# Optimization experiments

Hardware: AMD Instinct MI355X
Metric: run time of the kernel (lower is better)

## Reference

```python
import jax, jax.numpy as jnp
import numpy as np


def setup_inputs() -> dict:
    key = jax.random.key(0)
    k1, k2 = jax.random.split(key)
    inp = jax.random.normal(k1, (16, 64, 64, 64), dtype=jnp.float32)  # (B, D, H, W)
    codebook = jax.random.normal(k2, (1024, 64), dtype=jnp.float32)  # (K, D)
    return {"input": inp, "codebook": codebook}


def reference(input, codebook):
    # input: (B, D, *spatial); codebook: (K, D)
    B, D = input.shape[0], input.shape[1]
    spatial = input.shape[2:]
    # move channel dim last, flatten to tokens: (N, D)
    x = jnp.moveaxis(input, 1, -1).reshape(-1, D)
    # squared L2 distances (cdist^2), computed via expansion to avoid (N,K,D)
    x_sq = jnp.sum(x * x, axis=-1, keepdims=True)            # (N, 1)
    e_sq = jnp.sum(codebook * codebook, axis=-1)             # (K,)
    dist = x_sq - 2.0 * (x @ codebook.T) + e_sq              # (N, K)
    idx = jnp.argmin(dist, axis=-1)                          # (N,)
    quantized = jnp.take(codebook, idx, axis=0)              # (N, D)
    # reshape back to (B, *spatial, D) then move D to axis 1
    out = jnp.moveaxis(quantized.reshape((B,) + spatial + (D,)), -1, 1)
    indices = idx.reshape((B,) + spatial)
    return out, indices
```

## Files before the change

kernel.cpp:

```cpp
#include <hip/hip_runtime.h>


typedef _Float16 v8h  __attribute__((ext_vector_type(8)));
typedef float    v16f __attribute__((ext_vector_type(16)));

constexpr int   D         = 64;
constexpr int   K         = 1024;
constexpr int   HW        = 4096;
constexpr int   DHW       = D * HW;
constexpr int   OUT_ELEMS = 16 * DHW;
constexpr float EPS       = 0.04f;


__global__ __launch_bounds__(256) void vq_prep(
    const float* __restrict__ cb, _Float16* __restrict__ CH, float* __restrict__ esq)
{
    const int blk = blockIdx.x, tid = threadIdx.x;
    if (blk < 72) {
        const int gid  = blk * 256 + tid;
        const int lane = gid & 63;
        const int fid  = gid >> 6;
        const int t    = fid / 9;
        const int kc   = fid - 9 * t;
        const int l31  = lane & 31;
        const int lh   = lane >> 5;
        const int cw   = t * 32 + l31;
        v8h h;
        if (kc < 8) {
            const int  kk = kc & 3;
            const bool lo = kc >= 4;
            const float* src = cb + cw * D + kk * 16 + lh * 8;
            #pragma unroll
            for (int j = 0; j < 8; ++j) {
                const float v = -2.0f * src[j];
                const _Float16 vh = (_Float16)v;
                h[j] = lo ? (_Float16)(v - (float)vh) : vh;
            }
        } else {
            #pragma unroll
            for (int j = 0; j < 8; ++j) h[j] = (_Float16)0.0f;
            if (lh == 0) {
                const float4* c4 = (const float4*)(cb + cw * D);
                float a0 = 0.f, a1 = 0.f, a2 = 0.f, a3 = 0.f;
                #pragma unroll
                for (int j = 0; j < 16; ++j) {
                    const float4 c = c4[j];
                    a0 = fmaf(c.x, c.x, a0);
                    a1 = fmaf(c.y, c.y, a1);
                    a2 = fmaf(c.z, c.z, a2);
                    a3 = fmaf(c.w, c.w, a3);
                }
                const float e = (a0 + a1) + (a2 + a3);
                const _Float16 ehi = (_Float16)e;
                h[0] = ehi;
                h[1] = (_Float16)(e - (float)ehi);
            }
        }
        *(v8h*)(CH + (size_t)fid * 512 + lane * 8) = h;
    } else {
        const int cw = (blk - 72) * 256 + tid;
        const float4* c4 = (const float4*)(cb + cw * D);
        float a0 = 0.f, a1 = 0.f, a2 = 0.f, a3 = 0.f;
        #pragma unroll
        for (int j = 0; j < 16; ++j) {
            const float4 c = c4[j];
            a0 = fmaf(c.x, c.x, a0);
            a1 = fmaf(c.y, c.y, a1);
            a2 = fmaf(c.z, c.z, a2);
            a3 = fmaf(c.w, c.w, a3);
        }
        esq[cw] = (a0 + a1) + (a2 + a3);
    }
}

__global__ __launch_bounds__(256, 3) void vq_scan(
    const float* __restrict__ input,
    const float* __restrict__ codebook,
    const _Float16* __restrict__ CH,
    const float* __restrict__ esq,
    float* __restrict__ out)
{
    __shared__ union {
        _Float16 bf[2][4][64][8];
        float    q[64][65];
    } u;
    __shared__ float    s_pv[4][64];
    __shared__ float    s_p2[4][64];
    __shared__ int      s_pk[4][64];
    __shared__ int      s_idx[64];
    __shared__ int      s_list[64];
    __shared__ int      s_cnt;
    __shared__ float    s_xf[64];
    __shared__ float    s_redv[4];
    __shared__ int      s_redk[4];

    const int tid  = threadIdx.x;
    const int lane = tid & 63;
    const int q    = __builtin_amdgcn_readfirstlane(tid >> 6);
    const int lh   = lane >> 5;
    const int tok0 = blockIdx.x * 64;
    const int b    = tok0 >> 12;
    const int hwb  = tok0 & 4095;

    if (tid == 0) s_cnt = 0;

    {
        const float* xb = input + (size_t)b * DHW + hwb;
        #pragma unroll
        for (int pass = 0; pass < 4; ++pass) {
            const int d   = pass * 16 + (tid >> 4);
            const int hw4 = (tid & 15) * 4;
            const float4 v = *(const float4*)(xb + (size_t)d * HW + hw4);
            const float vv[4] = {v.x, v.y, v.z, v.w};
            #pragma unroll
            for (int uu = 0; uu < 4; ++uu) {
                const int tk = hw4 + uu;
                u.bf[tk >> 5][d >> 4][((d >> 3) & 1) * 32 + (tk & 31)][d & 7] =
                    (_Float16)vv[uu];
            }
        }
    }
    __syncthreads();

    v8h bh[2][4];
    #pragma unroll
    for (int ct = 0; ct < 2; ++ct)
        #pragma unroll
        for (int kc = 0; kc < 4; ++kc)
            bh[ct][kc] = *(const v8h*)&u.bf[ct][kc][lane][0];

    v8h b5;
    #pragma unroll
    for (int j = 0; j < 8; ++j) b5[j] = (_Float16)0.0f;
    if (lh == 0) { b5[0] = (_Float16)1.0f; b5[1] = (_Float16)1.0f; }

    v16f Z = {0,0,0,0,0,0,0,0,0,0,0,0,0,0,0,0};
    const float INF = __builtin_huge_valf();
    float bv0 = INF, b20 = INF, bv1 = INF, b21 = INF;
    int   sl0 = 0, sl1 = 0;

    const v8h* Abase = (const v8h*)CH + lane;

    #pragma unroll 2
    for (int t = 0; t < 8; ++t) {
        const v8h* Ap = Abase + (size_t)((q * 8 + t) * 9) * 64;
        v8h ah[4], al[4];
        #pragma unroll
        for (int kc = 0; kc < 4; ++kc) {
            ah[kc] = Ap[kc * 64];
            al[kc] = Ap[(kc + 4) * 64];
        }
        const v8h ae = Ap[512];

        v16f acc0 = __builtin_amdgcn_mfma_f32_32x32x16_f16(ae, b5, Z, 0, 0, 0);
        v16f acc1 = __builtin_amdgcn_mfma_f32_32x32x16_f16(ae, b5, Z, 0, 0, 0);

        #pragma unroll
        for (int kc = 0; kc < 4; ++kc) {
            acc0 = __builtin_amdgcn_mfma_f32_32x32x16_f16(ah[kc], bh[0][kc], acc0, 0, 0, 0);
            acc1 = __builtin_amdgcn_mfma_f32_32x32x16_f16(ah[kc], bh[1][kc], acc1, 0, 0, 0);
        }
        #pragma unroll
        for (int kc = 0; kc < 4; ++kc) {
            acc0 = __builtin_amdgcn_mfma_f32_32x32x16_f16(al[kc], bh[0][kc], acc0, 0, 0, 0);
            acc1 = __builtin_amdgcn_mfma_f32_32x32x16_f16(al[kc], bh[1][kc], acc1, 0, 0, 0);
        }

        #pragma unroll
        for (int r = 0; r < 16; ++r) {
            const int slot = (t << 4) | r;
            const float s0 = acc0[r];
            b20 = __builtin_amdgcn_fmed3f(s0, bv0, b20);
            if (s0 < bv0) { bv0 = s0; sl0 = slot; }
            const float s1 = acc1[r];
            b21 = __builtin_amdgcn_fmed3f(s1, bv1, b21);
            if (s1 < bv1) { bv1 = s1; sl1 = slot; }
        }
    }

    #pragma unroll
    for (int ct = 0; ct < 2; ++ct) {
        const float bv = ct ? bv1 : bv0;
        const float b2 = ct ? b21 : b20;
        const int   sl = ct ? sl1 : sl0;
        const float obv = __shfl_xor(bv, 32, 64);
        const float ob2 = __shfl_xor(b2, 32, 64);
        const int   osl = __shfl_xor(sl, 32, 64);
        const bool  oth = obv < bv;
        const float B1  = oth ? obv : bv;
        const float B2  = fminf(fmaxf(bv, obv), fminf(b2, ob2));
        const int   wsl = oth ? osl : sl;
        const int   wlh = oth ? (lh ^ 1) : lh;
        const int   r   = wsl & 15;
        const int   tt  = wsl >> 4;
        const int   cw  = (q * 8 + tt) * 32 + (r & 3) + 8 * (r >> 2) + 4 * wlh;
        if (lane < 32) {
            s_pv[q][ct * 32 + lane] = B1;
            s_p2[q][ct * 32 + lane] = B2;
            s_pk[q][ct * 32 + lane] = cw;
        }
    }
    __syncthreads();

    if (tid < 64) {
        float B1 = INF, B2 = INF; int CW = 0;
        #pragma unroll
        for (int qq = 0; qq < 4; ++qq) {
            const float pv = s_pv[qq][tid];
            const float p2 = s_p2[qq][tid];
            const int   pk = s_pk[qq][tid];
            if (pv < B1) { B2 = fminf(B1, p2); B1 = pv; CW = pk; }
            else         { B2 = fminf(B2, pv); }
        }
        s_idx[tid] = CW;
        if (B2 - B1 < EPS) {
            const int p = atomicAdd(&s_cnt, 1);
            s_list[p] = tid;
        }
    }
    __syncthreads();

    {
        const int cnt = s_cnt;
        const int rr  = tid >> 2;
        const int c   = tid & 3;
        for (int ii = 0; ii < cnt; ++ii) {
            const int tl = s_list[ii];
            if (tid < 64) s_xf[tid] = input[(size_t)b * DHW + (size_t)tid * HW + (hwb + tl)];
            __syncthreads();
            const float4* xs4 = (const float4*)&s_xf[c * 16];
            const float4 x0 = xs4[0], x1 = xs4[1], x2 = xs4[2], x3 = xs4[3];
            float bestv = INF; int bestk = K;
            #pragma unroll 4
            for (int i = 0; i < 16; ++i) {
                const int k = i * 64 + rr;
                const float4* c4 = (const float4*)(codebook + (size_t)k * D + c * 16);
                const float4 c0 = c4[0], c1 = c4[1], c2 = c4[2], c3 = c4[3];
                float p0 = 0.f, p1 = 0.f, p2 = 0.f, p3 = 0.f;
                p0 = fmaf(x0.x, c0.x, p0); p0 = fmaf(x0.y, c0.y, p0);
                p0 = fmaf(x0.z, c0.z, p0); p0 = fmaf(x0.w, c0.w, p0);
                p1 = fmaf(x1.x, c1.x, p1); p1 = fmaf(x1.y, c1.y, p1);
                p1 = fmaf(x1.z, c1.z, p1); p1 = fmaf(x1.w, c1.w, p1);
                p2 = fmaf(x2.x, c2.x, p2); p2 = fmaf(x2.y, c2.y, p2);
                p2 = fmaf(x2.z, c2.z, p2); p2 = fmaf(x2.w, c2.w, p2);
                p3 = fmaf(x3.x, c3.x, p3); p3 = fmaf(x3.y, c3.y, p3);
                p3 = fmaf(x3.z, c3.z, p3); p3 = fmaf(x3.w, c3.w, p3);
                float dp = (p0 + p1) + (p2 + p3);
                dp += __shfl_xor(dp, 1, 64);
                dp += __shfl_xor(dp, 2, 64);
                const float s = fmaf(-2.0f, dp, esq[k]);
                if (s < bestv) { bestv = s; bestk = k; }
            }
            #pragma unroll
            for (int off = 4; off <= 32; off <<= 1) {
                const float ov = __shfl_xor(bestv, off, 64);
                const int   ok = __shfl_xor(bestk, off, 64);
                if (ov < bestv || (ov == bestv && ok < bestk)) { bestv = ov; bestk = ok; }
            }
            if (lane == 0) { s_redv[q] = bestv; s_redk[q] = bestk; }
            __syncthreads();
            if (tid == 0) {
                float bb = s_redv[0]; int bk = s_redk[0];
                #pragma unroll
                for (int w = 1; w < 4; ++w) {
                    const float v = s_redv[w]; const int kk = s_redk[w];
                    if (v < bb || (v == bb && kk < bk)) { bb = v; bk = kk; }
                }
                s_idx[tl] = bk;
            }
            __syncthreads();
        }
    }

    {
        const int rs  = tid >> 2;
        const int c   = tid & 3;
        const int idx = s_idx[rs];
        const float4* src = (const float4*)(codebook + (size_t)idx * D + c * 16);
        #pragma unroll
        for (int j = 0; j < 4; ++j) {
            const float4 v = src[j];
            float* dst = &u.q[rs][c * 16 + j * 4];
            dst[0] = v.x; dst[1] = v.y; dst[2] = v.z; dst[3] = v.w;
        }
    }
    __syncthreads();
    {
        float* ob = out + (size_t)b * DHW + hwb;
        #pragma unroll
        for (int pass = 0; pass < 4; ++pass) {
            const int d   = pass * 16 + (tid >> 4);
            const int hw4 = (tid & 15) * 4;
            float4 v;
            v.x = u.q[hw4 + 0][d];
            v.y = u.q[hw4 + 1][d];
            v.z = u.q[hw4 + 2][d];
            v.w = u.q[hw4 + 3][d];
            *(float4*)(ob + (size_t)d * HW + hw4) = v;
        }
        if (tid < 64) out[OUT_ELEMS + tok0 + tid] = (float)s_idx[tid];
    }
}

extern "C" void kernel_launch(void* const* d_in, const int* in_sizes, int n_in,
                              void* d_out, int out_size, void* d_ws, size_t ws_size,
                              hipStream_t stream) {
    const float* input    = (const float*)d_in[0];
    const float* codebook = (const float*)d_in[1];
    float* out            = (float*)d_out;

    _Float16* CH  = (_Float16*)d_ws;
    float*    esq = (float*)((char*)d_ws + 294912);

    vq_prep<<<76, 256, 0, stream>>>(codebook, CH, esq);
    vq_scan<<<1024, 256, 0, stream>>>(input, codebook, CH, esq, out);
}
```

Before: 120.1 us.

## Double token tile per block, software-pipeline codebook loads, per-wave fallback rescoring

Each scan block now handles 128 tokens instead of 64, so every codebook fragment loaded from global memory feeds four MFMA column groups instead of two, halving codebook traffic per token. The codebook A-fragment loads are double-buffered across tile iterations to overlap with the MFMA work. The exact fp32 fallback for ambiguous tokens now gives each wave its own token with no block-wide barriers per token, and prep folds the esq computation into the fragment pass. The cost is higher register and LDS use, with occupancy hint lowered to 2 blocks per CU and half as many blocks launched.

```diff
diff --git a/kernel.cpp b/kernel.cpp
--- a/kernel.cpp
+++ b/kernel.cpp
@@ -15,65 +15,50 @@
 __global__ __launch_bounds__(256) void vq_prep(
     const float* __restrict__ cb, _Float16* __restrict__ CH, float* __restrict__ esq)
 {
-    const int blk = blockIdx.x, tid = threadIdx.x;
-    if (blk < 72) {
-        const int gid  = blk * 256 + tid;
-        const int lane = gid & 63;
-        const int fid  = gid >> 6;
-        const int t    = fid / 9;
-        const int kc   = fid - 9 * t;
-        const int l31  = lane & 31;
-        const int lh   = lane >> 5;
-        const int cw   = t * 32 + l31;
-        v8h h;
-        if (kc < 8) {
-            const int  kk = kc & 3;
-            const bool lo = kc >= 4;
-            const float* src = cb + cw * D + kk * 16 + lh * 8;
-            #pragma unroll
-            for (int j = 0; j < 8; ++j) {
-                const float v = -2.0f * src[j];
-                const _Float16 vh = (_Float16)v;
-                h[j] = lo ? (_Float16)(v - (float)vh) : vh;
-            }
-        } else {
-            #pragma unroll
-            for (int j = 0; j < 8; ++j) h[j] = (_Float16)0.0f;
-            if (lh == 0) {
-                const float4* c4 = (const float4*)(cb + cw * D);
-                float a0 = 0.f, a1 = 0.f, a2 = 0.f, a3 = 0.f;
-                #pragma unroll
-                for (int j = 0; j < 16; ++j) {
-                    const float4 c = c4[j];
-                    a0 = fmaf(c.x, c.x, a0);
-                    a1 = fmaf(c.y, c.y, a1);
-                    a2 = fmaf(c.z, c.z, a2);
-                    a3 = fmaf(c.w, c.w, a3);
-                }
-                const float e = (a0 + a1) + (a2 + a3);
-                const _Float16 ehi = (_Float16)e;
-                h[0] = ehi;
-                h[1] = (_Float16)(e - (float)ehi);
-            }
-        }
-        *(v8h*)(CH + (size_t)fid * 512 + lane * 8) = h;
+    const int gid  = blockIdx.x * 256 + threadIdx.x;
+    const int lane = gid & 63;
+    const int fid  = gid >> 6;
+    const int t    = fid / 9;
+    const int kc   = fid - 9 * t;
+    const int l31  = lane & 31;
+    const int lh   = lane >> 5;
+    const int cw   = t * 32 + l31;
+    v8h h;
+    if (kc < 8) {
+        const int  kk = kc & 3;
+        const bool lo = kc >= 4;
+        const float* src = cb + cw * D + kk * 16 + lh * 8;
+        #pragma unroll
+        for (int j = 0; j < 8; ++j) {
+            const float v = -2.0f * src[j];
+            const _Float16 vh = (_Float16)v;
+            h[j] = lo ? (_Float16)(v - (float)vh) : vh;
+        }
     } else {
-        const int cw = (blk - 72) * 256 + tid;
-        const float4* c4 = (const float4*)(cb + cw * D);
-        float a0 = 0.f, a1 = 0.f, a2 = 0.f, a3 = 0.f;
-        #pragma unroll
-        for (int j = 0; j < 16; ++j) {
-            const float4 c = c4[j];
-            a0 = fmaf(c.x, c.x, a0);
-            a1 = fmaf(c.y, c.y, a1);
-            a2 = fmaf(c.z, c.z, a2);
-            a3 = fmaf(c.w, c.w, a3);
-        }
-        esq[cw] = (a0 + a1) + (a2 + a3);
-    }
+        #pragma unroll
+        for (int j = 0; j < 8; ++j) h[j] = (_Float16)0.0f;
+        if (lh == 0) {
+            const float4* c4 = (const float4*)(cb + cw * D);
+            float a0 = 0.f, a1 = 0.f, a2 = 0.f, a3 = 0.f;
+            #pragma unroll
+            for (int j = 0; j < 16; ++j) {
+                const float4 c = c4[j];
+                a0 = fmaf(c.x, c.x, a0);
+                a1 = fmaf(c.y, c.y, a1);
+                a2 = fmaf(c.z, c.z, a2);
+                a3 = fmaf(c.w, c.w, a3);
+            }
+            const float e = (a0 + a1) + (a2 + a3);
+            const _Float16 ehi = (_Float16)e;
+            h[0] = ehi;
+            h[1] = (_Float16)(e - (float)ehi);
+            esq[cw] = e;
+        }
+    }
+    *(v8h*)(CH + (size_t)fid * 512 + lane * 8) = h;
 }
 
-__global__ __launch_bounds__(256, 3) void vq_scan(
+__global__ __launch_bounds__(256, 2) void vq_scan(
     const float* __restrict__ input,
     const float* __restrict__ codebook,
     const _Float16* __restrict__ CH,
@@ -81,24 +66,22 @@
     float* __restrict__ out)
 {
     __shared__ union {
-        _Float16 bf[2][4][64][8];
-        float    q[64][65];
+        _Float16 bf[4][4][64][8];
+        float    q[128][65];
     } u;
-    __shared__ float    s_pv[4][64];
-    __shared__ float    s_p2[4][64];
-    __shared__ int      s_pk[4][64];
-    __shared__ int      s_idx[64];
-    __shared__ int      s_list[64];
-    __shared__ int      s_cnt;
-    __shared__ float    s_xf[64];
-    __shared__ float    s_redv[4];
-    __shared__ int      s_redk[4];
+    __shared__ float s_pv[4][128];
+    __shared__ float s_p2[4][128];
+    __shared__ int   s_pk[4][128];
+    __shared__ int   s_idx[128];
+    __shared__ int   s_list[128];
+    __shared__ int   s_cnt;
+    __shared__ float s_xf[4][64];
 
     const int tid  = threadIdx.x;
     const int lane = tid & 63;
     const int q    = __builtin_amdgcn_readfirstlane(tid >> 6);
     const int lh   = lane >> 5;
-    const int tok0 = blockIdx.x * 64;
+    const int tok0 = blockIdx.x * 128;
     const int b    = tok0 >> 12;
     const int hwb  = tok0 & 4095;
 
@@ -107,14 +90,14 @@
     {
         const float* xb = input + (size_t)b * DHW + hwb;
         #pragma unroll
-        for (int pass = 0; pass < 4; ++pass) {
-            const int d   = pass * 16 + (tid >> 4);
-            const int hw4 = (tid & 15) * 4;
-            const float4 v = *(const float4*)(xb + (size_t)d * HW + hw4);
+        for (int pass = 0; pass < 8; ++pass) {
+            const int d   = pass * 8 + (tid >> 5);
+            const int tk4 = (tid & 31) * 4;
+            const float4 v = *(const float4*)(xb + (size_t)d * HW + tk4);
             const float vv[4] = {v.x, v.y, v.z, v.w};
             #pragma unroll
             for (int uu = 0; uu < 4; ++uu) {
-                const int tk = hw4 + uu;
+                const int tk = tk4 + uu;
                 u.bf[tk >> 5][d >> 4][((d >> 3) & 1) * 32 + (tk & 31)][d & 7] =
                     (_Float16)vv[uu];
             }
@@ -122,12 +105,12 @@
     }
     __syncthreads();
 
-    v8h bh[2][4];
+    v8h bh[4][4];
     #pragma unroll
-    for (int ct = 0; ct < 2; ++ct)
+    for (int g = 0; g < 4; ++g)
         #pragma unroll
         for (int kc = 0; kc < 4; ++kc)
-            bh[ct][kc] = *(const v8h*)&u.bf[ct][kc][lane][0];
+            bh[g][kc] = *(const v8h*)&u.bf[g][kc][lane][0];
 
     v8h b5;
     #pragma unroll
@@ -136,73 +119,82 @@
 
     v16f Z = {0,0,0,0,0,0,0,0,0,0,0,0,0,0,0,0};
     const float INF = __builtin_huge_valf();
-    float bv0 = INF, b20 = INF, bv1 = INF, b21 = INF;
-    int   sl0 = 0, sl1 = 0;
+    float bv[4] = {INF, INF, INF, INF};
+    float b2[4] = {INF, INF, INF, INF};
+    int   sl[4] = {0, 0, 0, 0};
 
     const v8h* Abase = (const v8h*)CH + lane;
 
-    #pragma unroll 2
-    for (int t = 0; t < 8; ++t) {
+    v8h ah0[4], al0[4], ae0, ah1[4], al1[4], ae1;
+
+    auto loadA = [&](int t, v8h (&ah)[4], v8h (&al)[4], v8h& ae) {
         const v8h* Ap = Abase + (size_t)((q * 8 + t) * 9) * 64;
-        v8h ah[4], al[4];
         #pragma unroll
         for (int kc = 0; kc < 4; ++kc) {
             ah[kc] = Ap[kc * 64];
             al[kc] = Ap[(kc + 4) * 64];
         }
-        const v8h ae = Ap[512];
-
-        v16f acc0 = __builtin_amdgcn_mfma_f32_32x32x16_f16(ae, b5, Z, 0, 0, 0);
-        v16f acc1 = __builtin_amdgcn_mfma_f32_32x32x16_f16(ae, b5, Z, 0, 0, 0);
-
-        #pragma unroll
-        for (int kc = 0; kc < 4; ++kc) {
-            acc0 = __builtin_amdgcn_mfma_f32_32x32x16_f16(ah[kc], bh[0][kc], acc0, 0, 0, 0);
-            acc1 = __builtin_amdgcn_mfma_f32_32x32x16_f16(ah[kc], bh[1][kc], acc1, 0, 0, 0);
-        }
-        #pragma unroll
-        for (int kc = 0; kc < 4; ++kc) {
-            acc0 = __builtin_amdgcn_mfma_f32_32x32x16_f16(al[kc], bh[0][kc], acc0, 0, 0, 0);
-            acc1 = __builtin_amdgcn_mfma_f32_32x32x16_f16(al[kc], bh[1][kc], acc1, 0, 0, 0);
-        }
-
+        ae = Ap[512];
+    };
+
+    auto tile = [&](int t, const v8h (&ah)[4], const v8h (&al)[4], const v8h& ae) {
+        v16f acc[4];
+        #pragma unroll
+        for (int g = 0; g < 4; ++g)
+            acc[g] = __builtin_amdgcn_mfma_f32_32x32x16_f16(ae, b5, Z, 0, 0, 0);
+        #pragma unroll
+        for (int kc = 0; kc < 4; ++kc)
+            #pragma unroll
+            for (int g = 0; g < 4; ++g)
+                acc[g] = __builtin_amdgcn_mfma_f32_32x32x16_f16(ah[kc], bh[g][kc], acc[g], 0, 0, 0);
+        #pragma unroll
+        for (int kc = 0; kc < 4; ++kc)
+            #pragma unroll
+            for (int g = 0; g < 4; ++g)
+                acc[g] = __builtin_amdgcn_mfma_f32_32x32x16_f16(al[kc], bh[g][kc], acc[g], 0, 0, 0);
         #pragma unroll
         for (int r = 0; r < 16; ++r) {
             const int slot = (t << 4) | r;
-            const float s0 = acc0[r];
-            b20 = __builtin_amdgcn_fmed3f(s0, bv0, b20);
-            if (s0 < bv0) { bv0 = s0; sl0 = slot; }
-            const float s1 = acc1[r];
-            b21 = __builtin_amdgcn_fmed3f(s1, bv1, b21);
-            if (s1 < bv1) { bv1 = s1; sl1 = slot; }
-        }
+            #pragma unroll
+            for (int g = 0; g < 4; ++g) {
+                const float s = acc[g][r];
+                b2[g] = __builtin_amdgcn_fmed3f(s, bv[g], b2[g]);
+                if (s < bv[g]) { bv[g] = s; sl[g] = slot; }
+            }
+        }
+    };
+
+    loadA(0, ah0, al0, ae0);
+    #pragma unroll 1
+    for (int t = 0; t < 8; t += 2) {
+        loadA(t + 1, ah1, al1, ae1);
+        tile(t, ah0, al0, ae0);
+        if (t + 2 < 8) loadA(t + 2, ah0, al0, ae0);
+        tile(t + 1, ah1, al1, ae1);
     }
 
     #pragma unroll
-    for (int ct = 0; ct < 2; ++ct) {
-        const float bv = ct ? bv1 : bv0;
-        const float b2 = ct ? b21 : b20;
-        const int   sl = ct ? sl1 : sl0;
-        const float obv = __shfl_xor(bv, 32, 64);
-        const float ob2 = __shfl_xor(b2, 32, 64);
-        const int   osl = __shfl_xor(sl, 32, 64);
-        const bool  oth = obv < bv;
-        const float B1  = oth ? obv : bv;
-        const float B2  = fminf(fmaxf(bv, obv), fminf(b2, ob2));
-        const int   wsl = oth ? osl : sl;
+    for (int g = 0; g < 4; ++g) {
+        const float obv = __shfl_xor(bv[g], 32, 64);
+        const float ob2 = __shfl_xor(b2[g], 32, 64);
+        const int   osl = __shfl_xor(sl[g], 32, 64);
+        const bool  oth = obv < bv[g];
+        const float B1  = oth ? obv : bv[g];
+        const float B2  = fminf(fmaxf(bv[g], obv), fminf(b2[g], ob2));
+        const int   wsl = oth ? osl : sl[g];
         const int   wlh = oth ? (lh ^ 1) : lh;
         const int   r   = wsl & 15;
         const int   tt  = wsl >> 4;
         const int   cw  = (q * 8 + tt) * 32 + (r & 3) + 8 * (r >> 2) + 4 * wlh;
         if (lane < 32) {
-            s_pv[q][ct * 32 + lane] = B1;
-            s_p2[q][ct * 32 + lane] = B2;
-            s_pk[q][ct * 32 + lane] = cw;
-        }
-    }
-    __syncthreads();
-
-    if (tid < 64) {
+            s_pv[q][g * 32 + lane] = B1;
+            s_p2[q][g * 32 + lane] = B2;
+            s_pk[q][g * 32 + lane] = cw;
+        }
+    }
+    __syncthreads();
+
+    if (tid < 128) {
         float B1 = INF, B2 = INF; int CW = 0;
         #pragma unroll
         for (int qq = 0; qq < 4; ++qq) {
@@ -222,65 +214,52 @@
 
     {
         const int cnt = s_cnt;
-        const int rr  = tid >> 2;
-        const int c   = tid & 3;
-        for (int ii = 0; ii < cnt; ++ii) {
+        for (int ii = q; ii < cnt; ii += 4) {
             const int tl = s_list[ii];
-            if (tid < 64) s_xf[tid] = input[(size_t)b * DHW + (size_t)tid * HW + (hwb + tl)];
-            __syncthreads();
-            const float4* xs4 = (const float4*)&s_xf[c * 16];
-            const float4 x0 = xs4[0], x1 = xs4[1], x2 = xs4[2], x3 = xs4[3];
-            float bestv = INF; int bestk = K;
+            s_xf[q][lane] = input[(size_t)b * DHW + (size_t)lane * HW + (hwb + tl)];
+            float dot[16];
+            #pragma unroll
+            for (int i = 0; i < 16; ++i) dot[i] = 0.f;
             #pragma unroll 4
+            for (int dc = 0; dc < 16; ++dc) {
+                const float4 x4 = *(const float4*)&s_xf[q][dc * 4];
+                #pragma unroll
+                for (int i = 0; i < 16; ++i) {
+                    const int k = i * 64 + lane;
+                    const float4 c4 = *(const float4*)(codebook + (size_t)k * D + dc * 4);
+                    dot[i] = fmaf(x4.x, c4.x, dot[i]);
+                    dot[i] = fmaf(x4.y, c4.y, dot[i]);
+                    dot[i] = fmaf(x4.z, c4.z, dot[i]);
+                    dot[i] = fmaf(x4.w, c4.w, dot[i]);
+                }
+            }
+            float bestv = INF; int bestk = 0x7fffffff;
+            #pragma unroll
             for (int i = 0; i < 16; ++i) {
-                const int k = i * 64 + rr;
-                const float4* c4 = (const float4*)(codebook + (size_t)k * D + c * 16);
-                const float4 c0 = c4[0], c1 = c4[1], c2 = c4[2], c3 = c4[3];
-                float p0 = 0.f, p1 = 0.f, p2 = 0.f, p3 = 0.f;
-                p0 = fmaf(x0.x, c0.x, p0); p0 = fmaf(x0.y, c0.y, p0);
-                p0 = fmaf(x0.z, c0.z, p0); p0 = fmaf(x0.w, c0.w, p0);
-                p1 = fmaf(x1.x, c1.x, p1); p1 = fmaf(x1.y, c1.y, p1);
-                p1 = fmaf(x1.z, c1.z, p1); p1 = fmaf(x1.w, c1.w, p1);
-                p2 = fmaf(x2.x, c2.x, p2); p2 = fmaf(x2.y, c2.y, p2);
-                p2 = fmaf(x2.z, c2.z, p2); p2 = fmaf(x2.w, c2.w, p2);
-                p3 = fmaf(x3.x, c3.x, p3); p3 = fmaf(x3.y, c3.y, p3);
-                p3 = fmaf(x3.z, c3.z, p3); p3 = fmaf(x3.w, c3.w, p3);
-                float dp = (p0 + p1) + (p2 + p3);
-                dp += __shfl_xor(dp, 1, 64);
-                dp += __shfl_xor(dp, 2, 64);
-                const float s = fmaf(-2.0f, dp, esq[k]);
+                const int k = i * 64 + lane;
+                const float s = fmaf(-2.0f, dot[i], esq[k]);
                 if (s < bestv) { bestv = s; bestk = k; }
             }
             #pragma unroll
-            for (int off = 4; off <= 32; off <<= 1) {
+            for (int off = 1; off < 64; off <<= 1) {
                 const float ov = __shfl_xor(bestv, off, 64);
                 const int   ok = __shfl_xor(bestk, off, 64);
                 if (ov < bestv || (ov == bestv && ok < bestk)) { bestv = ov; bestk = ok; }
             }
-            if (lane == 0) { s_redv[q] = bestv; s_redk[q] = bestk; }
-            __syncthreads();
-            if (tid == 0) {
-                float bb = s_redv[0]; int bk = s_redk[0];
-                #pragma unroll
-                for (int w = 1; w < 4; ++w) {
-                    const float v = s_redv[w]; const int kk = s_redk[w];
-                    if (v < bb || (v == bb && kk < bk)) { bb = v; bk = kk; }
-                }
-                s_idx[tl] = bk;
-            }
-            __syncthreads();
-        }
-    }
-
-    {
-        const int rs  = tid >> 2;
-        const int c   = tid & 3;
+            if (lane == 0) s_idx[tl] = bestk;
+        }
+    }
+    __syncthreads();
+
+    {
+        const int rs  = tid >> 1;
+        const int c   = tid & 1;
         const int idx = s_idx[rs];
-        const float4* src = (const float4*)(codebook + (size_t)idx * D + c * 16);
-        #pragma unroll
-        for (int j = 0; j < 4; ++j) {
+        const float4* src = (const float4*)(codebook + (size_t)idx * D + c * 32);
+        #pragma unroll
+        for (int j = 0; j < 8; ++j) {
             const float4 v = src[j];
-            float* dst = &u.q[rs][c * 16 + j * 4];
+            float* dst = &u.q[rs][c * 32 + j * 4];
             dst[0] = v.x; dst[1] = v.y; dst[2] = v.z; dst[3] = v.w;
         }
     }
@@ -288,17 +267,17 @@
     {
         float* ob = out + (size_t)b * DHW + hwb;
         #pragma unroll
-        for (int pass = 0; pass < 4; ++pass) {
-            const int d   = pass * 16 + (tid >> 4);
-            const int hw4 = (tid & 15) * 4;
+        for (int pass = 0; pass < 8; ++pass) {
+            const int d   = pass * 8 + (tid >> 5);
+            const int tk4 = (tid & 31) * 4;
             float4 v;
-            v.x = u.q[hw4 + 0][d];
-            v.y = u.q[hw4 + 1][d];
-            v.z = u.q[hw4 + 2][d];
-            v.w = u.q[hw4 + 3][d];
-            *(float4*)(ob + (size_t)d * HW + hw4) = v;
-        }
-        if (tid < 64) out[OUT_ELEMS + tok0 + tid] = (float)s_idx[tid];
+            v.x = u.q[tk4 + 0][d];
+            v.y = u.q[tk4 + 1][d];
+            v.z = u.q[tk4 + 2][d];
+            v.w = u.q[tk4 + 3][d];
+            *(float4*)(ob + (size_t)d * HW + tk4) = v;
+        }
+        if (tid < 128) out[OUT_ELEMS + tok0 + tid] = (float)s_idx[tid];
     }
 }
 
@@ -312,6 +291,6 @@
     _Float16* CH  = (_Float16*)d_ws;
     float*    esq = (float*)((char*)d_ws + 294912);
 
-    vq_prep<<<76, 256, 0, stream>>>(codebook, CH, esq);
-    vq_scan<<<1024, 256, 0, stream>>>(input, codebook, CH, esq, out);
+    vq_prep<<<72, 256, 0, stream>>>(codebook, CH, esq);
+    vq_scan<<<512, 256, 0, stream>>>(input, codebook, CH, esq, out);
 }
```

Measured after the change: 161.7 us. 34.6% more time.

## Fuse codebook prep into scan kernel and parallelize fallback rescoring per wave

Applied to the files above, without the earlier changes.

Removes the separate codebook preprocessing kernel. Each scan block now converts codebook rows to split fp16 hi/lo and computes the squared norms inline, with the -2 factor moved onto the input tile. The exact fp32 fallback for ambiguous tokens now gives each wave its own token and computes direct squared differences, with no block-wide barriers per token. This saves a launch and a workspace round trip, but every block redoes the fp16 conversion and norm work, and the fallback reads more codebook data per token.

```diff
diff --git a/kernel.cpp b/kernel.cpp
--- a/kernel.cpp
+++ b/kernel.cpp
@@ -11,88 +11,22 @@
 constexpr int   OUT_ELEMS = 16 * DHW;
 constexpr float EPS       = 0.04f;
 
-
-__global__ __launch_bounds__(256) void vq_prep(
-    const float* __restrict__ cb, _Float16* __restrict__ CH, float* __restrict__ esq)
-{
-    const int blk = blockIdx.x, tid = threadIdx.x;
-    if (blk < 72) {
-        const int gid  = blk * 256 + tid;
-        const int lane = gid & 63;
-        const int fid  = gid >> 6;
-        const int t    = fid / 9;
-        const int kc   = fid - 9 * t;
-        const int l31  = lane & 31;
-        const int lh   = lane >> 5;
-        const int cw   = t * 32 + l31;
-        v8h h;
-        if (kc < 8) {
-            const int  kk = kc & 3;
-            const bool lo = kc >= 4;
-            const float* src = cb + cw * D + kk * 16 + lh * 8;
-            #pragma unroll
-            for (int j = 0; j < 8; ++j) {
-                const float v = -2.0f * src[j];
-                const _Float16 vh = (_Float16)v;
-                h[j] = lo ? (_Float16)(v - (float)vh) : vh;
-            }
-        } else {
-            #pragma unroll
-            for (int j = 0; j < 8; ++j) h[j] = (_Float16)0.0f;
-            if (lh == 0) {
-                const float4* c4 = (const float4*)(cb + cw * D);
-                float a0 = 0.f, a1 = 0.f, a2 = 0.f, a3 = 0.f;
-                #pragma unroll
-                for (int j = 0; j < 16; ++j) {
-                    const float4 c = c4[j];
-                    a0 = fmaf(c.x, c.x, a0);
-                    a1 = fmaf(c.y, c.y, a1);
-                    a2 = fmaf(c.z, c.z, a2);
-                    a3 = fmaf(c.w, c.w, a3);
-                }
-                const float e = (a0 + a1) + (a2 + a3);
-                const _Float16 ehi = (_Float16)e;
-                h[0] = ehi;
-                h[1] = (_Float16)(e - (float)ehi);
-            }
-        }
-        *(v8h*)(CH + (size_t)fid * 512 + lane * 8) = h;
-    } else {
-        const int cw = (blk - 72) * 256 + tid;
-        const float4* c4 = (const float4*)(cb + cw * D);
-        float a0 = 0.f, a1 = 0.f, a2 = 0.f, a3 = 0.f;
-        #pragma unroll
-        for (int j = 0; j < 16; ++j) {
-            const float4 c = c4[j];
-            a0 = fmaf(c.x, c.x, a0);
-            a1 = fmaf(c.y, c.y, a1);
-            a2 = fmaf(c.z, c.z, a2);
-            a3 = fmaf(c.w, c.w, a3);
-        }
-        esq[cw] = (a0 + a1) + (a2 + a3);
-    }
-}
-
-__global__ __launch_bounds__(256, 3) void vq_scan(
+__global__ __launch_bounds__(256, 3) void vq_fused(
     const float* __restrict__ input,
     const float* __restrict__ codebook,
-    const _Float16* __restrict__ CH,
-    const float* __restrict__ esq,
     float* __restrict__ out)
 {
     __shared__ union {
         _Float16 bf[2][4][64][8];
         float    q[64][65];
     } u;
-    __shared__ float    s_pv[4][64];
-    __shared__ float    s_p2[4][64];
-    __shared__ int      s_pk[4][64];
-    __shared__ int      s_idx[64];
-    __shared__ int      s_list[64];
-    __shared__ int      s_cnt;
-    __shared__ float    s_xf[64];
-    __shared__ float    s_redv[4];
-    __shared__ int      s_redk[4];
+    __shared__ float s_pv[4][64];
+    __shared__ float s_p2[4][64];
+    __shared__ int   s_pk[4][64];
+    __shared__ int   s_idx[64];
+    __shared__ int   s_list[64];
+    __shared__ int   s_cnt;
+    __shared__ float s_xf[4][64];
 
     const int tid  = threadIdx.x;
     const int lane = tid & 63;
@@ -109,14 +43,14 @@
         #pragma unroll
         for (int pass = 0; pass < 4; ++pass) {
             const int d   = pass * 16 + (tid >> 4);
-            const int hw4 = (tid & 15) * 4;
-            const float4 v = *(const float4*)(xb + (size_t)d * HW + hw4);
+            const int tk4 = (tid & 15) * 4;
+            const float4 v = *(const float4*)(xb + (size_t)d * HW + tk4);
             const float vv[4] = {v.x, v.y, v.z, v.w};
             #pragma unroll
             for (int uu = 0; uu < 4; ++uu) {
-                const int tk = hw4 + uu;
+                const int tk = tk4 + uu;
                 u.bf[tk >> 5][d >> 4][((d >> 3) & 1) * 32 + (tk & 31)][d & 7] =
-                    (_Float16)vv[uu];
+                    (_Float16)(-2.0f * vv[uu]);
             }
         }
     }
@@ -139,22 +73,42 @@
     float bv0 = INF, b20 = INF, bv1 = INF, b21 = INF;
     int   sl0 = 0, sl1 = 0;
 
-    const v8h* Abase = (const v8h*)CH + lane;
-
-    #pragma unroll 2
+    #pragma unroll 1
     for (int t = 0; t < 8; ++t) {
-        const v8h* Ap = Abase + (size_t)((q * 8 + t) * 9) * 64;
+        const int row = (q * 8 + t) * 32 + (lane & 31);
+        const float* crow = codebook + (size_t)row * D + lh * 8;
+
         v8h ah[4], al[4];
+        float partial = 0.f;
         #pragma unroll
         for (int kc = 0; kc < 4; ++kc) {
-            ah[kc] = Ap[kc * 64];
-            al[kc] = Ap[(kc + 4) * 64];
-        }
-        const v8h ae = Ap[512];
+            const float4 c0 = *(const float4*)(crow + kc * 16);
+            const float4 c1 = *(const float4*)(crow + kc * 16 + 4);
+            const float cv[8] = {c0.x, c0.y, c0.z, c0.w, c1.x, c1.y, c1.z, c1.w};
+            v8h hi, lo;
+            #pragma unroll
+            for (int j = 0; j < 8; ++j) {
+                const float v  = cv[j];
+                const _Float16 vh = (_Float16)v;
+                hi[j] = vh;
+                lo[j] = (_Float16)(v - (float)vh);
+                partial = fmaf(v, v, partial);
+            }
+            ah[kc] = hi;
+            al[kc] = lo;
+        }
+        const float e = partial + __shfl_xor(partial, 32, 64);
+        v8h ae;
+        #pragma unroll
+        for (int j = 0; j < 8; ++j) ae[j] = (_Float16)0.0f;
+        if (lh == 0) {
+            const _Float16 eh = (_Float16)e;
+            ae[0] = eh;
+            ae[1] = (_Float16)(e - (float)eh);
+        }
 
         v16f acc0 = __builtin_amdgcn_mfma_f32_32x32x16_f16(ae, b5, Z, 0, 0, 0);
         v16f acc1 = __builtin_amdgcn_mfma_f32_32x32x16_f16(ae, b5, Z, 0, 0, 0);
-
         #pragma unroll
         for (int kc = 0; kc < 4; ++kc) {
             acc0 = __builtin_amdgcn_mfma_f32_32x32x16_f16(ah[kc], bh[0][kc], acc0, 0, 0, 0);
@@ -222,55 +176,45 @@
 
     {
         const int cnt = s_cnt;
-        const int rr  = tid >> 2;
-        const int c   = tid & 3;
-        for (int ii = 0; ii < cnt; ++ii) {
+        for (int ii = q; ii < cnt; ii += 4) {
             const int tl = s_list[ii];
-            if (tid < 64) s_xf[tid] = input[(size_t)b * DHW + (size_t)tid * HW + (hwb + tl)];
-            __syncthreads();
-            const float4* xs4 = (const float4*)&s_xf[c * 16];
-            const float4 x0 = xs4[0], x1 = xs4[1], x2 = xs4[2], x3 = xs4[3];
-            float bestv = INF; int bestk = K;
+            s_xf[q][lane] = input[(size_t)b * DHW + (size_t)lane * HW + (hwb + tl)];
+            float ss[16];
+            #pragma unroll
+            for (int i = 0; i < 16; ++i) ss[i] = 0.f;
             #pragma unroll 4
+            for (int dc = 0; dc < 16; ++dc) {
+                const float4 x4 = *(const float4*)&s_xf[q][dc * 4];
+                #pragma unroll
+                for (int i = 0; i < 16; ++i) {
+                    const int k = i * 64 + lane;
+                    const float4 c4 = *(const float4*)(codebook + (size_t)k * D + dc * 4);
+                    const float d0 = c4.x - x4.x;
+                    const float d1 = c4.y - x4.y;
+                    const float d2 = c4.z - x4.z;
+                    const float d3 = c4.w - x4.w;
+                    ss[i] = fmaf(d0, d0, ss[i]);
+                    ss[i] = fmaf(d1, d1, ss[i]);
+                    ss[i] = fmaf(d2, d2, ss[i]);
+                    ss[i] = fmaf(d3, d3, ss[i]);
+                }
+            }
+            float bestv = INF; int bestk = 0x7fffffff;
+            #pragma unroll
             for (int i = 0; i < 16; ++i) {
-                const int k = i * 64 + rr;
-                const float4* c4 = (const float4*)(codebook + (size_t)k * D + c * 16);
-                const float4 c0 = c4[0], c1 = c4[1], c2 = c4[2], c3 = c4[3];
-                float p0 = 0.f, p1 = 0.f, p2 = 0.f, p3 = 0.f;
-                p0 = fmaf(x0.x, c0.x, p0); p0 = fmaf(x0.y, c0.y, p0);
-                p0 = fmaf(x0.z, c0.z, p0); p0 = fmaf(x0.w, c0.w, p0);
-                p1 = fmaf(x1.x, c1.x, p1); p1 = fmaf(x1.y, c1.y, p1);
-                p1 = fmaf(x1.z, c1.z, p1); p1 = fmaf(x1.w, c1.w, p1);
-                p2 = fmaf(x2.x, c2.x, p2); p2 = fmaf(x2.y, c2.y, p2);
-                p2 = fmaf(x2.z, c2.z, p2); p2 = fmaf(x2.w, c2.w, p2);
-                p3 = fmaf(x3.x, c3.x, p3); p3 = fmaf(x3.y, c3.y, p3);
-                p3 = fmaf(x3.z, c3.z, p3); p3 = fmaf(x3.w, c3.w, p3);
-                float dp = (p0 + p1) + (p2 + p3);
-                dp += __shfl_xor(dp, 1, 64);
-                dp += __shfl_xor(dp, 2, 64);
-                const float s = fmaf(-2.0f, dp, esq[k]);
-                if (s < bestv) { bestv = s; bestk = k; }
-            }
-            #pragma unroll
-            for (int off = 4; off <= 32; off <<= 1) {
+                const int k = i * 64 + lane;
+                if (ss[i] < bestv) { bestv = ss[i]; bestk = k; }
+            }
+            #pragma unroll
+            for (int off = 1; off < 64; off <<= 1) {
                 const float ov = __shfl_xor(bestv, off, 64);
                 const int   ok = __shfl_xor(bestk, off, 64);
                 if (ov < bestv || (ov == bestv && ok < bestk)) { bestv = ov; bestk = ok; }
             }
-            if (lane == 0) { s_redv[q] = bestv; s_redk[q] = bestk; }
-            __syncthreads();
-            if (tid == 0) {
-                float bb = s_redv[0]; int bk = s_redk[0];
-                #pragma unroll
-                for (int w = 1; w < 4; ++w) {
-                    const float v = s_redv[w]; const int kk = s_redk[w];
-                    if (v < bb || (v == bb && kk < bk)) { bb = v; bk = kk; }
-                }
-                s_idx[tl] = bk;
-            }
-            __syncthreads();
-        }
-    }
+            if (lane == 0) s_idx[tl] = bestk;
+        }
+    }
+    __syncthreads();
 
     {
         const int rs  = tid >> 2;
@@ -290,13 +234,13 @@
         #pragma unroll
         for (int pass = 0; pass < 4; ++pass) {
             const int d   = pass * 16 + (tid >> 4);
-            const int hw4 = (tid & 15) * 4;
+            const int tk4 = (tid & 15) * 4;
             float4 v;
-            v.x = u.q[hw4 + 0][d];
-            v.y = u.q[hw4 + 1][d];
-            v.z = u.q[hw4 + 2][d];
-            v.w = u.q[hw4 + 3][d];
-            *(float4*)(ob + (size_t)d * HW + hw4) = v;
+            v.x = u.q[tk4 + 0][d];
+            v.y = u.q[tk4 + 1][d];
+            v.z = u.q[tk4 + 2][d];
+            v.w = u.q[tk4 + 3][d];
+            *(float4*)(ob + (size_t)d * HW + tk4) = v;
         }
         if (tid < 64) out[OUT_ELEMS + tok0 + tid] = (float)s_idx[tid];
     }
@@ -308,10 +252,7 @@
     const float* input    = (const float*)d_in[0];
     const float* codebook = (const float*)d_in[1];
     float* out            = (float*)d_out;
-
-    _Float16* CH  = (_Float16*)d_ws;
-    float*    esq = (float*)((char*)d_ws + 294912);
-
-    vq_prep<<<76, 256, 0, stream>>>(codebook, CH, esq);
-    vq_scan<<<1024, 256, 0, stream>>>(input, codebook, CH, esq, out);
+    (void)d_ws; (void)ws_size;
+
+    vq_fused<<<1024, 256, 0, stream>>>(input, codebook, out);
 }
```

After: 186.0 us. 54.8% more time.
